# Kernel optimization log

Measured on AMD Instinct MI355X. Metric: run time of the kernel, lower is better.

The kernel has to match this reference:

```python
import jax, jax.numpy as jnp
import numpy as np

THRESHOLD = 0.005
EPS = 1e-5  # torch instance_norm default eps


def setup_inputs() -> dict:
    key = jax.random.key(0)
    k1, k2, k3 = jax.random.split(key, 3)
    B, C, H, W = 4, 64, 64, 64
    feat = 64
    stdv = 1.0 / np.sqrt(feat)  # matches __init_W_bias__ uniform(-stdv, stdv)
    x = jax.random.normal(k1, (B, C, H, W), dtype=jnp.float32)
    W0 = jax.random.uniform(k2, (1, feat, feat), dtype=jnp.float32, minval=-stdv, maxval=stdv)
    W1 = jax.random.uniform(k3, (1, feat, feat), dtype=jnp.float32, minval=-stdv, maxval=stdv)
    return {"x": x, "W0": W0, "W1": W1}


def _laplacian(xn):
    # xn: [B, N, C] node features (pixels x channels). Built under no_grad in torch.
    norms = jnp.sqrt(jnp.sum(xn * xn, axis=2, keepdims=True))  # [B, N, 1]
    num = jnp.einsum('bnc,bmc->bnm', xn, xn)                    # [B, N, N]
    corr = num / (norms * jnp.swapaxes(norms, 1, 2))
    # relu then threshold -> binary adjacency (threshold > 0, so relu is subsumed)
    A = (corr > THRESHOLD).astype(xn.dtype)
    deg = jnp.sum(A, axis=2)                                    # [B, N]
    d_is = 1.0 / jnp.sqrt(deg)                                  # inverse(sqrt(D)) is diagonal
    return A * d_is[:, :, None] * d_is[:, None, :]              # D^-1/2 A D^-1/2


def _instance_norm(h):
    # torch F.instance_norm on [B, N, F] normalizes over the last dim per (b, n)
    mean = jnp.mean(h, axis=-1, keepdims=True)
    var = jnp.mean((h - mean) ** 2, axis=-1, keepdims=True)
    return (h - mean) / jnp.sqrt(var + EPS)


def reference(x, W0, W1):
    B, C, H, Wd = x.shape
    x_linear = x.reshape(B, C, H * Wd).transpose(0, 2, 1)  # [B, N, C]
    lap = _laplacian(jax.lax.stop_gradient(x_linear))       # adjacency built with no_grad
    for Wk in (W0, W1):
        lx = jnp.einsum('bnm,bmc->bnc', lap, x_linear)      # laplacian diffusion
        h = jnp.einsum('bnc,cf->bnf', lx, Wk[0])            # shared weight (repeat over batch)
        x_linear = jax.nn.relu(_instance_norm(h))
    return x_linear
```

## Files before the change

### kernel.cpp

```cpp
#include <hip/hip_runtime.h>
#include <hip/hip_bf16.h>
#include <cstdint>

#define BB 4
#define CC 64
#define NN 4096
#define NWRD 64
#define TAU 0.005f
#define EPSN 1e-5f
#define MSPLITS 8

typedef __attribute__((ext_vector_type(8))) short short8;
typedef __attribute__((ext_vector_type(4))) float f32x4;
typedef unsigned long long ull;

__device__ inline unsigned int bf16_rne(float v) {
    unsigned int u = __float_as_uint(v);
    return (u + 0x7FFFu + ((u >> 16) & 1u)) >> 16;
}

__device__ inline void gload_lds16(const void* g, void* lds_base) {
    __builtin_amdgcn_global_load_lds(
        (const __attribute__((address_space(1))) unsigned int*)g,
        (__attribute__((address_space(3))) unsigned int*)lds_base, 16, 0, 0);
}

__global__ __launch_bounds__(256) void k_transpose(const float* __restrict__ x,
                                                   float* __restrict__ xt,
                                                   unsigned short* __restrict__ ynh,
                                                   unsigned short* __restrict__ ynl,
                                                   int* __restrict__ deg) {
    __shared__ float lds[64 * 65];
    int t = threadIdx.x;
    int b = blockIdx.y;
    int n0 = blockIdx.x * 64;
    int gid = (b * (NN / 64) + blockIdx.x) * 256 + t;
    if (gid < BB * NN) deg[gid] = 0;
    #pragma unroll
    for (int i = 0; i < 4; ++i) {
        int c = i * 16 + (t >> 4);
        int nc = (t & 15) * 4;
        float4 v = *(const float4*)(x + ((size_t)(b * CC + c)) * NN + n0 + nc);
        lds[c * 65 + nc + 0] = v.x;
        lds[c * 65 + nc + 1] = v.y;
        lds[c * 65 + nc + 2] = v.z;
        lds[c * 65 + nc + 3] = v.w;
    }
    __syncthreads();
    int l = t & 63, wv = t >> 6;
    for (int i = 0; i < 16; ++i) {
        int n = wv * 16 + i;
        float v = lds[l * 65 + n];
        float s = v * v;
        #pragma unroll
        for (int off = 32; off; off >>= 1) s += __shfl_xor(s, off, 64);
        float yv = v * rsqrtf(s);
        unsigned int hb = bf16_rne(yv);
        float lo = yv - __uint_as_float(hb << 16);
        unsigned int lb = bf16_rne(lo);
        size_t row = (size_t)(b * NN + n0 + n);
        xt[row * CC + l] = v;
        ynh[row * CC + l] = (unsigned short)hb;
        ynl[row * CC + l] = (unsigned short)lb;
    }
}

#define CORR_MC 128
__global__ __launch_bounds__(256) void k_corr(const unsigned short* __restrict__ ynh,
                                              const unsigned short* __restrict__ ynl,
                                              ull* __restrict__ mask,
                                              int* __restrict__ deg) {
    __shared__ unsigned short ldsH[2][CORR_MC * 64];
    __shared__ unsigned short ldsL[2][CORR_MC * 64];
    int t = threadIdx.x;
    int l = t & 63, wv = t >> 6;
    int lc = l & 15, q = l >> 4;
    int b = blockIdx.z;
    int idx = blockIdx.x, I = 0;
    while (idx >= 16 - I) { idx -= 16 - I; ++I; }
    int J = I + idx;
    int n0 = I * 256 + wv * 64;
    int m0 = J * 256;
    const unsigned short* bH = ynh + (size_t)b * NN * CC;
    const unsigned short* bL = ynl + (size_t)b * NN * CC;

    short8 ah[4][2], al[4][2];
    #pragma unroll
    for (int nt = 0; nt < 4; ++nt)
        #pragma unroll
        for (int ks = 0; ks < 2; ++ks) {
            size_t off = (size_t)(n0 + nt * 16 + lc) * CC + (ks * 4 + q) * 8;
            ah[nt][ks] = *(const short8*)(bH + off);
            al[nt][ks] = *(const short8*)(bL + off);
        }

    int rr = l & 15;
    int rsel = rr & 3;
    int qq = rr >> 2;
    int myq = l >> 4;

    auto stage = [&](int mc, int bufi) {
        int mbase = m0 + mc * CORR_MC;
        #pragma unroll
        for (int rd = 0; rd < 4; ++rd) {
            int gu = rd * 256 + wv * 64;
            int g = gu + l;
            int ci = (g & ~7) | ((g & 7) ^ ((g >> 3) & 7));
            gload_lds16(bH + (size_t)mbase * CC + ci * 8, &ldsH[bufi][gu * 8]);
            gload_lds16(bL + (size_t)mbase * CC + ci * 8, &ldsL[bufi][gu * 8]);
        }
    };

    ull wout[4];
    int degacc = 0;
    stage(0, 0);
    for (int mc = 0; mc < 2; ++mc) {
        __syncthreads();
        if (mc == 0) stage(1, 1);
        int bufi = mc & 1;
        ull w0 = 0, w1 = 0;
        #pragma unroll
        for (int tt = 0; tt < 8; ++tt) {
            short8 bh[2], bl[2];
            #pragma unroll
            for (int ks = 0; ks < 2; ++ks) {
                int rowm = tt * 16 + lc;
                int sw = ((ks * 4 + q) ^ (rowm & 7)) * 8;
                bh[ks] = *(const short8*)&ldsH[bufi][rowm * 64 + sw];
                bl[ks] = *(const short8*)&ldsL[bufi][rowm * 64 + sw];
            }
            #pragma unroll
            for (int nt = 0; nt < 4; ++nt) {
                f32x4 acc = {0.f, 0.f, 0.f, 0.f};
                #pragma unroll
                for (int ks = 0; ks < 2; ++ks) {
                    acc = __builtin_amdgcn_mfma_f32_16x16x32_bf16(ah[nt][ks], bh[ks], acc, 0, 0, 0);
                    acc = __builtin_amdgcn_mfma_f32_16x16x32_bf16(ah[nt][ks], bl[ks], acc, 0, 0, 0);
                    acc = __builtin_amdgcn_mfma_f32_16x16x32_bf16(al[nt][ks], bh[ks], acc, 0, 0, 0);
                }
                ull bal[4];
                #pragma unroll
                for (int r = 0; r < 4; ++r)
                    bal[r] = __ballot(acc[r] > TAU);
                ull sa = (rsel & 1) ? bal[1] : bal[0];
                ull sb = (rsel & 1) ? bal[3] : bal[2];
                ull sel = (rsel & 2) ? sb : sa;
                ull part = ((sel >> (qq * 16)) & 0xFFFFull) << ((tt & 3) * 16);
                if (myq == nt) { if (tt < 4) w0 |= part; else w1 |= part; }
            }
        }
        wout[mc * 2 + 0] = w0;
        wout[mc * 2 + 1] = w1;
        degacc += __popcll(w0) + __popcll(w1);
    }

    int row = b * NN + n0 + l;
    ull* mdst = mask + (size_t)row * NWRD + J * 4;
    #pragma unroll
    for (int c = 0; c < 4; ++c) mdst[c] = wout[c];
    atomicAdd(&deg[row], degacc);

    if (J > I) {
        __syncthreads();
        ull* sh = (ull*)&ldsH[0][0];
        #pragma unroll
        for (int c = 0; c < 4; ++c) sh[(wv * 64 + l) * 5 + c] = wout[c];
        __syncthreads();
        const ull Mv[6] = {0x00000000FFFFFFFFull, 0x0000FFFF0000FFFFull,
                           0x00FF00FF00FF00FFull, 0x0F0F0F0F0F0F0F0Full,
                           0x3333333333333333ull, 0x5555555555555555ull};
        int dm = 0;
        ull tw[4];
        #pragma unroll
        for (int a = 0; a < 4; ++a) {
            ull xv = sh[(a * 64 + l) * 5 + wv];
            int dd = 32;
            #pragma unroll
            for (int s = 0; s < 6; ++s, dd >>= 1) {
                ull y = __shfl_xor(xv, dd, 64);
                ull M = Mv[s];
                xv = (l & dd) ? ((xv & ~M) | ((y >> dd) & M))
                              : ((xv & M) | ((y << dd) & ~M));
            }
            tw[a] = xv;
            dm += __popcll(xv);
        }
        int mrow = b * NN + J * 256 + wv * 64 + l;
        #pragma unroll
        for (int a = 0; a < 4; ++a)
            mask[(size_t)mrow * NWRD + I * 4 + a] = tw[a];
        atomicAdd(&deg[mrow], dm);
    }
}

__global__ __launch_bounds__(256) void k_pack(const float* __restrict__ xin,
                                              const int* __restrict__ deg,
                                              unsigned short* __restrict__ yph) {
    __shared__ float lds[32 * 65];
    int t = threadIdx.x;
    int kt = blockIdx.x;
    int b = blockIdx.y;
    size_t ibase = (size_t)b * NN * CC + (size_t)kt * 32 * CC;
    #pragma unroll
    for (int i = 0; i < 2; ++i) {
        int f4 = i * 256 + t;
        int m = f4 >> 4;
        float d = rsqrtf((float)deg[b * NN + kt * 32 + m]);
        float4 v = ((const float4*)(xin + ibase))[f4];
        int c = (f4 & 15) * 4;
        lds[m * 65 + c + 0] = v.x * d;
        lds[m * 65 + c + 1] = v.y * d;
        lds[m * 65 + c + 2] = v.z * d;
        lds[m * 65 + c + 3] = v.w * d;
    }
    __syncthreads();
    size_t obase = (size_t)b * NN * CC + (size_t)kt * 2048;
    int kin = t & 31;
    int chi = t >> 5;
    #pragma unroll
    for (int cg = 0; cg < 8; ++cg) {
        int c = cg * 8 + chi;
        yph[obase + c * 32 + kin] = (unsigned short)bf16_rne(lds[kin * 65 + c]);
    }
}

#define GMC 128
__global__ __launch_bounds__(256) void k_gemm(const ull* __restrict__ mask,
                                              const unsigned short* __restrict__ yph,
                                              float* __restrict__ plx) {
    __shared__ unsigned short ldsB[2][4 * 2048];
    int t = threadIdx.x;
    int l = t & 63, wv = t >> 6;
    int lc = l & 15, q = l >> 4;
    int b = blockIdx.z;
    int ms = blockIdx.y;
    int n0 = blockIdx.x * 256 + wv * 64;
    int m0 = ms * 512;
    const unsigned short* src = yph + (size_t)b * NN * CC;

    ull mw[4][4][2];
    #pragma unroll
    for (int nt = 0; nt < 4; ++nt) {
        const ull* mrow = mask + ((size_t)(b * NN + n0 + nt * 16 + lc)) * NWRD + (m0 >> 6);
        #pragma unroll
        for (int mc = 0; mc < 4; ++mc) {
            mw[mc][nt][0] = mrow[mc * 2];
            mw[mc][nt][1] = mrow[mc * 2 + 1];
        }
    }

    f32x4 acc[4][4];
    #pragma unroll
    for (int nt = 0; nt < 4; ++nt)
        #pragma unroll
        for (int tt = 0; tt < 4; ++tt) acc[nt][tt] = f32x4{0.f, 0.f, 0.f, 0.f};

    auto stage = [&](int mc, int bufi) {
        int ktbase = (m0 + mc * GMC) >> 5;
        #pragma unroll
        for (int rd = 0; rd < 4; ++rd) {
            int gu = rd * 256 + wv * 64;
            gload_lds16(src + (size_t)ktbase * 2048 + (gu + l) * 8, &ldsB[bufi][gu * 8]);
        }
    };

    stage(0, 0);
    for (int mc = 0; mc < 4; ++mc) {
        __syncthreads();
        if (mc + 1 < 4) stage(mc + 1, (mc + 1) & 1);
        int bufi = mc & 1;
        #pragma unroll
        for (int kt = 0; kt < 4; ++kt) {
            int sh = (kt & 1) * 32 + q * 8;
            union { unsigned int u[4]; short8 v; } a[4];
            #pragma unroll
            for (int nt = 0; nt < 4; ++nt) {
                unsigned int bits = (unsigned int)(mw[mc][nt][kt >> 1] >> sh) & 0xFFu;
                #pragma unroll
                for (int j = 0; j < 4; ++j)
                    a[nt].u[j] = ((bits >> (2 * j)) & 1u ? 0x3F80u : 0u)
                               | ((bits >> (2 * j + 1)) & 1u ? 0x3F800000u : 0u);
            }
            #pragma unroll
            for (int tt = 0; tt < 4; ++tt) {
                short8 bf = *(const short8*)&ldsB[bufi][kt * 2048 + (tt * 16 + lc) * 32 + q * 8];
                #pragma unroll
                for (int nt = 0; nt < 4; ++nt)
                    acc[nt][tt] = __builtin_amdgcn_mfma_f32_16x16x32_bf16(a[nt].v, bf, acc[nt][tt], 0, 0, 0);
            }
        }
    }
    #pragma unroll
    for (int nt = 0; nt < 4; ++nt)
        #pragma unroll
        for (int tt = 0; tt < 4; ++tt)
            #pragma unroll
            for (int r = 0; r < 4; ++r) {
                int n = n0 + nt * 16 + q * 4 + r;
                int c = tt * 16 + lc;
                plx[((size_t)((ms * BB + b)) * NN + n) * CC + c] = acc[nt][tt][r];
            }
}

__global__ __launch_bounds__(256) void k_out(const float* __restrict__ plx,
                                             const int* __restrict__ deg,
                                             const float* __restrict__ W,
                                             float* __restrict__ xout,
                                             unsigned short* __restrict__ xpack) {
    __shared__ float lxs[4][68];
    int lane = threadIdx.x & 63;
    int wave = threadIdx.x >> 6;
    int b = blockIdx.y;
    int n0 = blockIdx.x * 16 + wave * 4;
    float Wreg[64];
    #pragma unroll
    for (int c = 0; c < 64; ++c) Wreg[c] = W[c * 64 + lane];
    for (int tI = 0; tI < 4; ++tI) {
        int n = n0 + tI;
        size_t row = (size_t)(b * NN + n);
        float dRow = rsqrtf((float)deg[row]);
        float lx = 0.f;
        #pragma unroll
        for (int s = 0; s < MSPLITS; ++s)
            lx += plx[((size_t)(s * BB + b) * NN + n) * CC + lane];
        lx *= dRow;
        lxs[wave][lane] = lx;
        float h = 0.f;
        #pragma unroll
        for (int c4 = 0; c4 < 16; ++c4) {
            float4 s4 = *(const float4*)&lxs[wave][c4 * 4];
            h += s4.x * Wreg[c4 * 4 + 0] + s4.y * Wreg[c4 * 4 + 1]
               + s4.z * Wreg[c4 * 4 + 2] + s4.w * Wreg[c4 * 4 + 3];
        }
        float mean = h;
        #pragma unroll
        for (int off = 32; off; off >>= 1) mean += __shfl_xor(mean, off, 64);
        mean *= (1.f / 64.f);
        float dv = h - mean;
        float var = dv * dv;
        #pragma unroll
        for (int off = 32; off; off >>= 1) var += __shfl_xor(var, off, 64);
        var *= (1.f / 64.f);
        float o = dv * rsqrtf(var + EPSN);
        o = o > 0.f ? o : 0.f;
        if (xout)
            xout[row * CC + lane] = o;
        if (xpack)
            xpack[(size_t)b * NN * CC + (size_t)(n >> 5) * 2048 + lane * 32 + (n & 31)] =
                (unsigned short)bf16_rne(o * dRow);
    }
}

extern "C" void kernel_launch(void* const* d_in, const int* in_sizes, int n_in,
                              void* d_out, int out_size, void* d_ws, size_t ws_size,
                              hipStream_t stream) {
    const float* x  = (const float*)d_in[0];
    const float* W0 = (const float*)d_in[1];
    const float* W1 = (const float*)d_in[2];
    float* out = (float*)d_out;

    char* ws = (char*)d_ws;
    ull* mask = (ull*)(ws);
    float* xt = (float*)(ws + ((size_t)8 << 20));
    unsigned short* ynh = (unsigned short*)(ws + ((size_t)12 << 20));
    unsigned short* ynl = (unsigned short*)(ws + ((size_t)14 << 20));
    unsigned short* xp0 = (unsigned short*)(ws + ((size_t)16 << 20));
    unsigned short* xp1 = (unsigned short*)(ws + ((size_t)18 << 20));
    float* plx = (float*)(ws + ((size_t)20 << 20));
    int* deg = (int*)(ws + ((size_t)52 << 20));

    k_transpose<<<dim3(NN / 64, BB), 256, 0, stream>>>(x, xt, ynh, ynl, deg);
    k_corr<<<dim3(136, 1, BB), 256, 0, stream>>>(ynh, ynl, mask, deg);

    k_pack<<<dim3(128, BB), 256, 0, stream>>>(xt, deg, xp0);
    k_gemm<<<dim3(NN / 256, MSPLITS, BB), 256, 0, stream>>>(mask, xp0, plx);
    k_out<<<dim3(NN / 16, BB), 256, 0, stream>>>(plx, deg, W0, nullptr, xp1);

    k_gemm<<<dim3(NN / 256, MSPLITS, BB), 256, 0, stream>>>(mask, xp1, plx);
    k_out<<<dim3(NN / 16, BB), 256, 0, stream>>>(plx, deg, W1, out, nullptr);
}
```

Before: 153.3 us.

## Fold column degree scaling into GEMM A-operand and drop pack kernel

The column-side D^-1/2 scaling moves from the packed B operand into the mask-expanded A operand: a bf16 dinv vector is ANDed with the expanded mask bits, so the B operand can be the raw bf16 features. This lets the transpose kernel write the packed bf16 layout directly, which removes the fp32 xt buffer and the separate k_pack launch. A small k_dinv kernel is added, and k_out no longer multiplies by dRow when packing. The costs are one extra vector load per k-tile in the GEMM and slightly different rounding, since dinv is now rounded to bf16 on its own.

```diff
diff --git a/kernel.cpp b/kernel.cpp
--- a/kernel.cpp
+++ b/kernel.cpp
@@ -26,7 +26,7 @@
 }
 
 __global__ __launch_bounds__(256) void k_transpose(const float* __restrict__ x,
-                                                   float* __restrict__ xt,
+                                                   unsigned short* __restrict__ xp0,
                                                    unsigned short* __restrict__ ynh,
                                                    unsigned short* __restrict__ ynl,
                                                    int* __restrict__ deg) {
@@ -58,10 +58,12 @@
         unsigned int hb = bf16_rne(yv);
         float lo = yv - __uint_as_float(hb << 16);
         unsigned int lb = bf16_rne(lo);
-        size_t row = (size_t)(b * NN + n0 + n);
-        xt[row * CC + l] = v;
+        int ng = n0 + n;
+        size_t row = (size_t)(b * NN + ng);
         ynh[row * CC + l] = (unsigned short)hb;
         ynl[row * CC + l] = (unsigned short)lb;
+        xp0[(size_t)b * NN * CC + (size_t)(ng >> 5) * 2048 + l * 32 + (ng & 31)] =
+            (unsigned short)bf16_rne(v);
     }
 }
 
@@ -193,40 +195,16 @@
     }
 }
 
-__global__ __launch_bounds__(256) void k_pack(const float* __restrict__ xin,
-                                              const int* __restrict__ deg,
-                                              unsigned short* __restrict__ yph) {
-    __shared__ float lds[32 * 65];
-    int t = threadIdx.x;
-    int kt = blockIdx.x;
-    int b = blockIdx.y;
-    size_t ibase = (size_t)b * NN * CC + (size_t)kt * 32 * CC;
-    #pragma unroll
-    for (int i = 0; i < 2; ++i) {
-        int f4 = i * 256 + t;
-        int m = f4 >> 4;
-        float d = rsqrtf((float)deg[b * NN + kt * 32 + m]);
-        float4 v = ((const float4*)(xin + ibase))[f4];
-        int c = (f4 & 15) * 4;
-        lds[m * 65 + c + 0] = v.x * d;
-        lds[m * 65 + c + 1] = v.y * d;
-        lds[m * 65 + c + 2] = v.z * d;
-        lds[m * 65 + c + 3] = v.w * d;
-    }
-    __syncthreads();
-    size_t obase = (size_t)b * NN * CC + (size_t)kt * 2048;
-    int kin = t & 31;
-    int chi = t >> 5;
-    #pragma unroll
-    for (int cg = 0; cg < 8; ++cg) {
-        int c = cg * 8 + chi;
-        yph[obase + c * 32 + kin] = (unsigned short)bf16_rne(lds[kin * 65 + c]);
-    }
+__global__ __launch_bounds__(256) void k_dinv(const int* __restrict__ deg,
+                                              unsigned short* __restrict__ dinvb) {
+    int gid = blockIdx.x * 256 + threadIdx.x;
+    dinvb[gid] = (unsigned short)bf16_rne(rsqrtf((float)deg[gid]));
 }
 
 #define GMC 128
 __global__ __launch_bounds__(256) void k_gemm(const ull* __restrict__ mask,
                                               const unsigned short* __restrict__ yph,
+                                              const unsigned short* __restrict__ dinvb,
                                               float* __restrict__ plx) {
     __shared__ unsigned short ldsB[2][4 * 2048];
     int t = threadIdx.x;
@@ -237,6 +215,7 @@
     int n0 = blockIdx.x * 256 + wv * 64;
     int m0 = ms * 512;
     const unsigned short* src = yph + (size_t)b * NN * CC;
+    const unsigned short* dvb = dinvb + (size_t)b * NN;
 
     ull mw[4][4][2];
     #pragma unroll
@@ -269,17 +248,22 @@
         __syncthreads();
         if (mc + 1 < 4) stage(mc + 1, (mc + 1) & 1);
         int bufi = mc & 1;
+        int mbase = m0 + mc * GMC;
         #pragma unroll
         for (int kt = 0; kt < 4; ++kt) {
             int sh = (kt & 1) * 32 + q * 8;
+            union { unsigned int u[4]; short8 v; } dvu;
+            dvu.v = *(const short8*)(dvb + mbase + kt * 32 + q * 8);
             union { unsigned int u[4]; short8 v; } a[4];
             #pragma unroll
             for (int nt = 0; nt < 4; ++nt) {
                 unsigned int bits = (unsigned int)(mw[mc][nt][kt >> 1] >> sh) & 0xFFu;
                 #pragma unroll
-                for (int j = 0; j < 4; ++j)
-                    a[nt].u[j] = ((bits >> (2 * j)) & 1u ? 0x3F80u : 0u)
-                               | ((bits >> (2 * j + 1)) & 1u ? 0x3F800000u : 0u);
+                for (int j = 0; j < 4; ++j) {
+                    unsigned int mexp = (((bits >> (2 * j)) & 1u) ? 0x0000FFFFu : 0u)
+                                      | (((bits >> (2 * j + 1)) & 1u) ? 0xFFFF0000u : 0u);
+                    a[nt].u[j] = dvu.u[j] & mexp;
+                }
             }
             #pragma unroll
             for (int tt = 0; tt < 4; ++tt) {
@@ -347,7 +331,7 @@
             xout[row * CC + lane] = o;
         if (xpack)
             xpack[(size_t)b * NN * CC + (size_t)(n >> 5) * 2048 + lane * 32 + (n & 31)] =
-                (unsigned short)bf16_rne(o * dRow);
+                (unsigned short)bf16_rne(o);
     }
 }
 
@@ -361,21 +345,21 @@
 
     char* ws = (char*)d_ws;
     ull* mask = (ull*)(ws);
-    float* xt = (float*)(ws + ((size_t)8 << 20));
-    unsigned short* ynh = (unsigned short*)(ws + ((size_t)12 << 20));
-    unsigned short* ynl = (unsigned short*)(ws + ((size_t)14 << 20));
-    unsigned short* xp0 = (unsigned short*)(ws + ((size_t)16 << 20));
-    unsigned short* xp1 = (unsigned short*)(ws + ((size_t)18 << 20));
-    float* plx = (float*)(ws + ((size_t)20 << 20));
-    int* deg = (int*)(ws + ((size_t)52 << 20));
-
-    k_transpose<<<dim3(NN / 64, BB), 256, 0, stream>>>(x, xt, ynh, ynl, deg);
+    unsigned short* ynh = (unsigned short*)(ws + ((size_t)8  << 20));
+    unsigned short* ynl = (unsigned short*)(ws + ((size_t)10 << 20));
+    unsigned short* xp0 = (unsigned short*)(ws + ((size_t)12 << 20));
+    unsigned short* xp1 = (unsigned short*)(ws + ((size_t)14 << 20));
+    float* plx = (float*)(ws + ((size_t)16 << 20));
+    int* deg = (int*)(ws + ((size_t)48 << 20));
+    unsigned short* dinvb = (unsigned short*)(ws + ((size_t)48 << 20) + ((size_t)64 << 10));
+
+    k_transpose<<<dim3(NN / 64, BB), 256, 0, stream>>>(x, xp0, ynh, ynl, deg);
     k_corr<<<dim3(136, 1, BB), 256, 0, stream>>>(ynh, ynl, mask, deg);
-
-    k_pack<<<dim3(128, BB), 256, 0, stream>>>(xt, deg, xp0);
-    k_gemm<<<dim3(NN / 256, MSPLITS, BB), 256, 0, stream>>>(mask, xp0, plx);
+    k_dinv<<<dim3(BB * NN / 256), 256, 0, stream>>>(deg, dinvb);
+
+    k_gemm<<<dim3(NN / 256, MSPLITS, BB), 256, 0, stream>>>(mask, xp0, dinvb, plx);
     k_out<<<dim3(NN / 16, BB), 256, 0, stream>>>(plx, deg, W0, nullptr, xp1);
 
-    k_gemm<<<dim3(NN / 256, MSPLITS, BB), 256, 0, stream>>>(mask, xp1, plx);
+    k_gemm<<<dim3(NN / 256, MSPLITS, BB), 256, 0, stream>>>(mask, xp1, dinvb, plx);
     k_out<<<dim3(NN / 16, BB), 256, 0, stream>>>(plx, deg, W1, out, nullptr);
 }
```

Result: slower. 161.2 us (+5.1%).
